# Optimization experiments

Hardware: AMD Instinct MI355X
Metric: run time of the kernel (lower is better)

Reference implementation:

```python
import jax, jax.numpy as jnp
import numpy as np

N_FFT = 1024
HOP = 256
N_MELS = 128
SR = 16000
EPS = 1e-6
S = 0.025
ALPHA = 0.98
DELTA = 2.0
R = 0.5


def make_mel_fb():
    # Faithful port of F2M._init_buffers (onesided=True)
    n_freq = N_FFT // 2 + 1
    f_max = SR // 2
    m_min = 0.0
    m_max = 2595.0 * np.log10(1.0 + f_max / 700.0)
    m_pts = np.linspace(m_min, m_max, N_MELS + 2)
    f_pts = 700.0 * (10.0 ** (m_pts / 2595.0) - 1.0)
    bins = np.floor((n_freq - 1) * 2 * f_pts / SR).astype(np.int64)
    fb = np.zeros((n_freq, N_MELS), dtype=np.float32)
    for m in range(1, N_MELS + 1):
        a, b, c = int(bins[m - 1]), int(bins[m]), int(bins[m + 1])
        if a != b:
            fb[a:b, m - 1] = (np.arange(a, b) - a) / (b - a)
        if b != c:
            fb[b:c, m - 1] = (c - np.arange(b, c)) / (c - b)
    return jnp.asarray(fb)


def setup_inputs() -> dict:
    key = jax.random.key(0)
    x = jax.random.normal(key, (32, 160000), dtype=jnp.float32)
    return {"x": x, "fb": make_mel_fb()}


def reference(x, fb):
    # torch.stft with center=True (default), rectangular window (window=None)
    pad = N_FFT // 2
    xp = jnp.pad(x, ((0, 0), (pad, pad)), mode="reflect")
    n_frames = (xp.shape[1] - N_FFT) // HOP + 1
    idx = jnp.arange(n_frames)[:, None] * HOP + jnp.arange(N_FFT)[None, :]
    frames = xp[:, idx]                       # [B, T, n_fft]
    spec = jnp.abs(jnp.fft.rfft(frames, axis=-1))   # magnitude, [B, T, F]
    mel = jnp.einsum("btf,fm->btm", spec, fb)       # [B, T, M]

    # PCEN EMA smoother: M_0 = x_0, M_t = (1-s) M_{t-1} + s x_t
    def step(m_prev, frame):
        m = (1.0 - S) * m_prev + S * frame
        return m, m

    x0 = mel[:, 0, :]                               # [B, M]
    _, ms = jax.lax.scan(step, x0, jnp.swapaxes(mel[:, 1:, :], 0, 1))
    M = jnp.concatenate([x0[:, None, :], jnp.swapaxes(ms, 0, 1)], axis=1)

    out = (mel / (M + EPS) ** ALPHA + DELTA) ** R - DELTA ** R
    return out
```

## Files before the change

### kernel.cpp

```cpp
#include <hip/hip_runtime.h>
#include <math.h>

#define NMELS   128
#define NFRAMES 626
#define NPAIRS  313
#define NBATCH  32
#define LSAMP   160000
#define NFREQ   513
#define PPB     2
#define NBLK    ((NPAIRS + PPB - 1) / PPB)
#define NCHUNK  NBLK

struct Bins { int v[NMELS + 2]; };

__device__ __forceinline__ int refl(int i) {
    if (i < 0) i = -i;
    else if (i >= LSAMP) i = 2 * LSAMP - 2 - i;
    return i;
}

__device__ __forceinline__ float2 cadd(float2 a, float2 b){return make_float2(a.x+b.x, a.y+b.y);}
__device__ __forceinline__ float2 csub(float2 a, float2 b){return make_float2(a.x-b.x, a.y-b.y);}
__device__ __forceinline__ float2 cmul(float2 a, float2 b){
    return make_float2(fmaf(a.x,b.x,-a.y*b.y), fmaf(a.x,b.y,a.y*b.x));
}
__device__ __forceinline__ float2 cmulnegi(float2 a){return make_float2(a.y, -a.x);}

__device__ __forceinline__ void dft16(float2* z) {
    const float2 W1 = make_float2( 0.92387953251f, -0.38268343236f);
    const float2 W2 = make_float2( 0.70710678119f, -0.70710678119f);
    const float2 W3 = make_float2( 0.38268343236f, -0.92387953251f);
    const float2 W6 = make_float2(-0.70710678119f, -0.70710678119f);
    const float2 W9 = make_float2(-0.92387953251f,  0.38268343236f);
    float2 g[16];
    #pragma unroll
    for (int q = 0; q < 4; q++) {
        float2 t0=z[q], t1=z[4+q], t2=z[8+q], t3=z[12+q];
        float2 A=cadd(t0,t2), B=csub(t0,t2), C=cadd(t1,t3), D=csub(t1,t3);
        g[q]    = cadd(A,C);
        g[4+q]  = make_float2(B.x + D.y, B.y - D.x);
        g[8+q]  = csub(A,C);
        g[12+q] = make_float2(B.x - D.y, B.y + D.x);
    }
    g[4+1] =cmul(g[4+1], W1); g[4+2] =cmul(g[4+2], W2); g[4+3] =cmul(g[4+3], W3);
    g[8+1] =cmul(g[8+1], W2); g[8+2] =cmulnegi(g[8+2]); g[8+3] =cmul(g[8+3], W6);
    g[12+1]=cmul(g[12+1],W3); g[12+2]=cmul(g[12+2],W6);  g[12+3]=cmul(g[12+3],W9);
    #pragma unroll
    for (int r = 0; r < 4; r++) {
        float2 t0=g[4*r], t1=g[4*r+1], t2=g[4*r+2], t3=g[4*r+3];
        float2 A=cadd(t0,t2), B=csub(t0,t2), C=cadd(t1,t3), D=csub(t1,t3);
        z[r]    = cadd(A,C);
        z[r+4]  = make_float2(B.x + D.y, B.y - D.x);
        z[r+8]  = csub(A,C);
        z[r+12] = make_float2(B.x - D.y, B.y + D.x);
    }
}

__device__ __forceinline__ void twpow(float2 w1, float2* tw) {
    tw[1] = w1;
    tw[2] = cmul(tw[1], tw[1]);
    tw[4] = cmul(tw[2], tw[2]);
    tw[8] = cmul(tw[4], tw[4]);
    tw[3] = cmul(tw[2], tw[1]);
    tw[5] = cmul(tw[4], tw[1]);
    tw[6] = cmul(tw[4], tw[2]);
    tw[7] = cmul(tw[4], tw[3]);
    #pragma unroll
    for (int k = 9; k < 16; k++) tw[k] = cmul(tw[8], tw[k-8]);
}

__device__ __forceinline__ void dft4v(const float2* t, float2* Z) {
    float2 A=cadd(t[0],t[2]), B=csub(t[0],t[2]), C=cadd(t[1],t[3]), D=csub(t[1],t[3]);
    Z[0] = cadd(A,C);
    Z[1] = make_float2(B.x + D.y, B.y - D.x);
    Z[2] = csub(A,C);
    Z[3] = make_float2(B.x - D.y, B.y + D.x);
}

__device__ __forceinline__ void emitmag(float* spec, int k, float2 Zk, float2 Zn) {
    float ar = Zk.x + Zn.x, ai = Zk.y - Zn.y;
    float br = Zk.y + Zn.y, bi = Zn.x - Zk.x;
    spec[k]         = 0.5f * sqrtf(ar*ar + ai*ai);
    spec[NFREQ + k] = 0.5f * sqrtf(br*br + bi*bi);
}

__global__ __launch_bounds__(128, 4)
void fft_mel_kernel(const float* __restrict__ x, float* __restrict__ mel,
                    float* __restrict__ S, Bins bins) {
    __shared__ float2 wbuf[PPB][1088];

    const int tid = threadIdx.x;
    const int w   = tid >> 6;
    const int u   = tid & 63;
    const int P   = blockIdx.x;
    const int b   = blockIdx.y;
    const int p   = P * PPB + w;

    float acc[4];

    if (p < NPAIRS) {
        float2* buf  = wbuf[w];
        float*  spec = (float*)&wbuf[w][0];

        const float* xb = x + (size_t)b * LSAMP;
        const int base = 512 * p - 512;
        if (base >= 0 && base + 1280 <= LSAMP) {
            const float4* xv4 = (const float4*)(xb + base);
            #pragma unroll
            for (int j = 0; j < 4; j++) {
                float4 v0 = xv4[64*j + u];
                float4 v1 = xv4[64*j + u + 64];
                const int i = 4 * (64*j + u);
                buf[i]   = make_float2(v0.x, v1.x);
                buf[i+1] = make_float2(v0.y, v1.y);
                buf[i+2] = make_float2(v0.z, v1.z);
                buf[i+3] = make_float2(v0.w, v1.w);
            }
        } else {
            #pragma unroll
            for (int j = 0; j < 16; j++) {
                const int i = 64 * j + u;
                buf[i] = make_float2(xb[refl(base + i)], xb[refl(base + i + 256)]);
            }
        }

        float2 z[16], tw[16];

        #pragma unroll
        for (int a = 0; a < 16; a++) z[a] = buf[64*a + u];
        dft16(z);
        {
            float s, c; __sincosf(-(float)M_PI * (float)u * (1.0f/512.0f), &s, &c);
            twpow(make_float2(c, s), tw);
            #pragma unroll
            for (int k = 1; k < 16; k++) z[k] = cmul(z[k], tw[k]);
        }
        #pragma unroll
        for (int k = 0; k < 16; k++) buf[17*u + k] = z[k];

        const int k1 = u >> 2, bp = u & 3;
        #pragma unroll
        for (int a = 0; a < 16; a++) z[a] = buf[68*a + 17*bp + k1];
        dft16(z);
        {
            float s, c; __sincosf(-(float)M_PI * (float)bp * (1.0f/32.0f), &s, &c);
            twpow(make_float2(c, s), tw);
            #pragma unroll
            for (int k = 1; k < 16; k++) z[k] = cmul(z[k], tw[k]);
        }
        #pragma unroll
        for (int k = 0; k < 16; k++) buf[68*k + 17*bp + k1] = z[k];

        const int cA0 = u;
        const int cB0 = (u == 0) ? 128 : 256 - u;
        const int cA1 = 64 + u;
        const int cB1 = 192 - u;
        float2 tA0[4], tB0[4], tA1[4], tB1[4];
        #pragma unroll
        for (int bq = 0; bq < 4; bq++) {
            tA0[bq] = buf[68*(cA0 >> 4) + 17*bq + (cA0 & 15)];
            tB0[bq] = buf[68*(cB0 >> 4) + 17*bq + (cB0 & 15)];
            tA1[bq] = buf[68*(cA1 >> 4) + 17*bq + (cA1 & 15)];
            tB1[bq] = buf[68*(cB1 >> 4) + 17*bq + (cB1 & 15)];
        }
        {
            float2 ZA[4], ZB[4];
            dft4v(tA0, ZA); dft4v(tB0, ZB);
            #pragma unroll
            for (int j = 0; j < 2; j++) {
                float2 znA = (u == 0) ? ZA[(4-j) & 3] : ZB[3-j];
                emitmag(spec, cA0 + 256*j, ZA[j], znA);
                float2 znB = (u == 0) ? ZB[3-j] : ZA[3-j];
                emitmag(spec, cB0 + 256*j, ZB[j], znB);
            }
            if (u == 0) emitmag(spec, 512, ZA[2], ZA[2]);
            dft4v(tA1, ZA); dft4v(tB1, ZB);
            #pragma unroll
            for (int j = 0; j < 2; j++) {
                emitmag(spec, cA1 + 256*j, ZA[j], ZB[3-j]);
                emitmag(spec, cB1 + 256*j, ZB[j], ZA[3-j]);
            }
        }

        const int r = u & 31, pf = u >> 5;
        const float* sp = spec + pf * NFREQ;
        #pragma unroll
        for (int i = 0; i < 4; i++) {
            const int mm = 32*i + r;
            const int a = bins.v[mm], bb = bins.v[mm+1], c = bins.v[mm+2];
            float a0 = 0.f;
            if (bb > a) {
                float s = 0.f;
                for (int f = a; f < bb; f++) s = fmaf(sp[f], (float)(f - a), s);
                a0 += s / (float)(bb - a);
            }
            if (c > bb) {
                float s = 0.f;
                for (int f = bb; f < c; f++) s = fmaf(sp[f], (float)(c - f), s);
                a0 += s / (float)(c - bb);
            }
            acc[i] = a0;
            mel[((size_t)b * NFRAMES + 2*p + pf) * NMELS + mm] = a0;
        }
    }
    __syncthreads();

    float* melst = (float*)&wbuf[1][0];
    if (p < NPAIRS) {
        const int r = u & 31, pf = u >> 5;
        const int fl = 2*w + pf;
        #pragma unroll
        for (int i = 0; i < 4; i++) melst[fl*NMELS + 32*i + r] = acc[i];
    }
    __syncthreads();

    {
        const int t0 = P * 4;
        const int nf = (NFRAMES - t0 < 4) ? NFRAMES - t0 : 4;
        float s = 0.f;
        for (int f = 0; f < nf; f++) {
            float v = melst[f*NMELS + tid];
            s = (t0 + f == 0) ? v : fmaf(0.975f, s, 0.025f * v);
        }
        S[((size_t)b * NCHUNK + P) * NMELS + tid] = s;
    }
}

__global__ __launch_bounds__(256)
void pcen_scan(const float* __restrict__ S, float* __restrict__ Mstart) {
    const int idx = blockIdx.x * 256 + threadIdx.x;
    const int m = idx & 127;
    const int b = idx >> 7;
    if (b >= NBATCH) return;

    float D4; { float d = 0.975f; d *= d; d *= d; D4 = d; }

    const size_t base = (size_t)b * NCHUNK * NMELS + m;
    float M = 0.f;
    #pragma unroll 8
    for (int c = 0; c < NCHUNK; c++) {
        Mstart[base + (size_t)c * NMELS] = M;
        M = fmaf(D4, M, S[base + (size_t)c * NMELS]);
    }
}

__global__ __launch_bounds__(128)
void pcen_out(const float* __restrict__ mel, const float* __restrict__ Mstart,
              float* __restrict__ out) {
    const int m = threadIdx.x;
    const int c = blockIdx.x;
    const int b = blockIdx.y;

    float M = Mstart[((size_t)b * NCHUNK + c) * NMELS + m];

    const int t0 = c * 4;
    const int tend = (t0 + 4 < NFRAMES) ? t0 + 4 : NFRAMES;
    const float* mp = mel + (size_t)b * NFRAMES * NMELS + m;
    float*       op = out + (size_t)b * NFRAMES * NMELS + m;
    #pragma unroll 4
    for (int t = t0; t < tend; t++) {
        float v = mp[(size_t)t * NMELS];
        M = (t == 0) ? v : fmaf(0.975f, M, 0.025f * v);
        float den = __powf(M + 1e-6f, 0.98f);
        op[(size_t)t * NMELS] = sqrtf(v / den + 2.0f) - 1.41421356237f;
    }
}

extern "C" void kernel_launch(void* const* d_in, const int* in_sizes, int n_in,
                              void* d_out, int out_size, void* d_ws, size_t ws_size,
                              hipStream_t stream) {
    const float* x  = (const float*)d_in[0];
    float* out = (float*)d_out;

    float* mel    = (float*)d_ws;
    float* S      = mel + (size_t)NBATCH * NFRAMES * NMELS;
    float* Mstart = S   + (size_t)NBATCH * NCHUNK * NMELS;

    Bins bins;
    {
        const double m_max = 2595.0 * log10(1.0 + 8000.0 / 700.0);
        const double step  = m_max / 129.0;
        for (int i = 0; i < NMELS + 2; i++) {
            double mv = (i == NMELS + 1) ? m_max : (double)i * step;
            double f  = 700.0 * (pow(10.0, mv / 2595.0) - 1.0);
            bins.v[i] = (int)floor((double)(NFREQ - 1) * 2.0 * f / 16000.0);
        }
    }

    dim3 grid1(NBLK, NBATCH);
    fft_mel_kernel<<<grid1, 128, 0, stream>>>(x, mel, S, bins);

    pcen_scan<<<(NBATCH * NMELS + 255) / 256, 256, 0, stream>>>(S, Mstart);

    dim3 grid3(NCHUNK, NBATCH);
    pcen_out<<<grid3, 128, 0, stream>>>(mel, Mstart, out);
}
```

Baseline: 128.7 us.

## Parallelize PCEN chunk scan across wavefront lanes with shuffle-based prefix scan

```diff
diff --git a/kernel.cpp b/kernel.cpp
--- a/kernel.cpp
+++ b/kernel.cpp
@@ -228,20 +228,39 @@
 
 __global__ __launch_bounds__(256)
 void pcen_scan(const float* __restrict__ S, float* __restrict__ Mstart) {
-    const int idx = blockIdx.x * 256 + threadIdx.x;
-    const int m = idx & 127;
-    const int b = idx >> 7;
-    if (b >= NBATCH) return;
-
-    float D4; { float d = 0.975f; d *= d; d *= d; D4 = d; }
+    const int tid  = threadIdx.x;
+    const int lane = tid & 63;
+    const int wid  = blockIdx.x * 4 + (tid >> 6);
+    const int m = wid & 127;
+    const int b = wid >> 7;
+
+    const float D4  = 0.975f * 0.975f * 0.975f * 0.975f;
+    const float D12 = D4 * D4 * D4;
 
     const size_t base = (size_t)b * NCHUNK * NMELS + m;
-    float M = 0.f;
-    #pragma unroll 8
-    for (int c = 0; c < NCHUNK; c++) {
-        Mstart[base + (size_t)c * NMELS] = M;
-        M = fmaf(D4, M, S[base + (size_t)c * NMELS]);
-    }
+    const int c0 = 3 * lane;
+    float s0 = (c0     < NCHUNK) ? S[base + (size_t)(c0    ) * NMELS] : 0.f;
+    float s1 = (c0 + 1 < NCHUNK) ? S[base + (size_t)(c0 + 1) * NMELS] : 0.f;
+    float s2 = (c0 + 2 < NCHUNK) ? S[base + (size_t)(c0 + 2) * NMELS] : 0.f;
+
+    float X = fmaf(D4, fmaf(D4, s0, s1), s2);
+
+    float w = D12;
+    #pragma unroll
+    for (int s = 1; s < 64; s <<= 1) {
+        float y = __shfl_up(X, s, 64);
+        if (lane >= s) X = fmaf(w, y, X);
+        w = w * w;
+    }
+    float E = __shfl_up(X, 1, 64);
+    if (lane == 0) E = 0.f;
+
+    float M0 = E;
+    float M1 = fmaf(D4, M0, s0);
+    float M2 = fmaf(D4, M1, s1);
+    if (c0     < NCHUNK) Mstart[base + (size_t)(c0    ) * NMELS] = M0;
+    if (c0 + 1 < NCHUNK) Mstart[base + (size_t)(c0 + 1) * NMELS] = M1;
+    if (c0 + 2 < NCHUNK) Mstart[base + (size_t)(c0 + 2) * NMELS] = M2;
 }
 
 __global__ __launch_bounds__(128)
@@ -290,7 +309,7 @@
     dim3 grid1(NBLK, NBATCH);
     fft_mel_kernel<<<grid1, 128, 0, stream>>>(x, mel, S, bins);
 
-    pcen_scan<<<(NBATCH * NMELS + 255) / 256, 256, 0, stream>>>(S, Mstart);
+    pcen_scan<<<1024, 256, 0, stream>>>(S, Mstart);
 
     dim3 grid3(NCHUNK, NBATCH);
     pcen_out<<<grid3, 128, 0, stream>>>(mel, Mstart, out);
```

New measurement: 123.1 us. -4.4%, faster.
